# Performance work log

Measured on AMD Instinct MI355X. Metric: run time of the kernel, lower is better.

The kernel has to match this reference:

```python
import jax, jax.numpy as jnp
import numpy as np

D = 256          # descriptor_dim
H = 4            # num heads in AttentionPropagation
DH = D // H
SCALE = 0.1      # hparams['scale_factor']
THR = 0.2        # hparams['match_threshold']
NAMES = ['GATs', 'self', 'cross'] * 4


def conv1d(x, w, b):
    # 1x1 Conv1d == per-position matmul. x:[b,c,n] w:[o,c] b:[o]
    return jnp.einsum('oc,bcn->bon', w, x) + b[None, :, None]


def instnorm(x, eps=1e-5):
    # torch InstanceNorm1d (affine=False): normalize over spatial dim per channel
    mu = jnp.mean(x, axis=2, keepdims=True)
    var = jnp.var(x, axis=2, keepdims=True)
    return (x - mu) * jax.lax.rsqrt(var + eps)


def linear_attention(q, k, v):
    # q:[b,dh,h,nq] k,v:[b,dh,h,ns]
    eps = 1e-6
    q = jax.nn.elu(q) + 1.0
    k = jax.nn.elu(k) + 1.0
    m = v.shape[3]
    v = v / m
    KV = jnp.einsum('bdhm,bqhm->bqdh', k, v)
    Z = 1.0 / (jnp.einsum('bdhm,bdh->bhm', q, k.sum(3)) + eps)
    return jnp.einsum('bdhm,bqdh,bhm->bqhm', q, KV, Z) * m


def mha(x, src, pw, pb, mw, mb):
    b, _, nq = x.shape
    ns = src.shape[2]
    q = conv1d(x, pw[0], pb[0]).reshape(b, DH, H, nq)
    k = conv1d(src, pw[1], pb[1]).reshape(b, DH, H, ns)
    v = conv1d(src, pw[2], pb[2]).reshape(b, DH, H, ns)
    o = linear_attention(q, k, v).reshape(b, D, nq)
    return conv1d(o, mw, mb)


def attn_prop(x, src, pw, pb, mw, mb, w1, b1, w2, b2):
    msg = mha(x, src, pw, pb, mw, mb)
    y = jnp.concatenate([x, msg], axis=1)           # [b, 2D, n]
    y = jax.nn.relu(instnorm(conv1d(y, w1, b1)))
    return conv1d(y, w2, b2)


def gat(d2d, d3d, W, a):
    # GraphAttentionLayer (OnePose): include_self=True, additional=False,
    # with_linear_transform=True, concat=True; dropout inactive at eval.
    # d2d:[b,D,n*L] d3d:[b,D,n]
    b, _, n = d3d.shape
    x2 = jnp.transpose(d2d, (0, 2, 1)).reshape(b, n, -1, D)   # [b,n,L,D]
    x3 = jnp.transpose(d3d, (0, 2, 1))                        # [b,n,D]
    x2 = jnp.concatenate([x3[:, :, None, :], x2], axis=2)     # include self -> L+1
    Wh2 = jnp.einsum('bnld,do->bnlo', x2, W)
    Wh3 = jnp.einsum('bnd,do->bno', x3, W)
    e = jax.nn.leaky_relu(
        jnp.einsum('bno,o->bn', Wh3, a[:D])[:, :, None]
        + jnp.einsum('bnlo,o->bnl', Wh2, a[D:]), 0.2)
    att = jax.nn.softmax(e, axis=-1)
    h = jnp.einsum('bnl,bnld->bnd', att, Wh2)
    return jnp.transpose(jax.nn.elu(h), (0, 2, 1))            # [b,D,n]


def gnn_and_scores(dq, d3, d2db, projw, projb, mergew, mergeb,
                   mlp1w, mlp1b, mlp2w, mlp2b, gatW, gata, finw, finb):
    gi = 0
    ai = 0
    for name in NAMES:
        if name == 'GATs':
            d3 = gat(d2db, d3, gatW[gi], gata[gi])
            gi += 1
        else:
            src0, src1 = (d3, dq) if name == 'cross' else (dq, d3)
            p = (projw[ai], projb[ai], mergew[ai], mergeb[ai],
                 mlp1w[ai], mlp1b[ai], mlp2w[ai], mlp2b[ai])
            dq = dq + attn_prop(dq, src0, *p)
            d3 = d3 + attn_prop(d3, src1, *p)
            ai += 1
    mq = conv1d(dq, finw, finb)
    md = conv1d(d3, finw, finb)
    mq = mq / jnp.maximum(jnp.linalg.norm(mq, axis=1, keepdims=True), 1e-12)
    md = md / jnp.maximum(jnp.linalg.norm(md, axis=1, keepdims=True), 1e-12)
    scores = jnp.einsum('bdn,bdm->bnm', mq, md) / SCALE
    conf = jax.nn.softmax(scores, axis=1) * jax.nn.softmax(scores, axis=2)
    return conf


def setup_inputs() -> dict:
    key = jax.random.key(0)
    ks = jax.random.split(key, 16)
    b, n1, n2, L = 2, 3072, 3072, 8
    s = 0.02
    f32 = jnp.float32
    return {
        'desc2d_query': jax.random.normal(ks[0], (b, D, n1), f32),
        'desc3d_db': jax.random.normal(ks[1], (b, D, n2), f32),
        'desc2d_db': jax.random.normal(ks[2], (b, D, n2 * L), f32),
        'projw': jax.random.normal(ks[3], (8, 3, D, D), f32) * s,
        'projb': jnp.zeros((8, 3, D), f32),
        'mergew': jax.random.normal(ks[4], (8, D, D), f32) * s,
        'mergeb': jnp.zeros((8, D), f32),
        'mlp1w': jax.random.normal(ks[5], (8, 2 * D, 2 * D), f32) * s,
        'mlp1b': jnp.zeros((8, 2 * D), f32),
        'mlp2w': jax.random.normal(ks[6], (8, D, 2 * D), f32) * s,
        'mlp2b': jnp.zeros((8, D), f32),
        'gatW': jax.random.normal(ks[7], (4, D, D), f32) * s,
        'gata': jax.random.normal(ks[8], (4, 2 * D), f32) * s,
        'finw': jax.random.normal(ks[9], (D, D), f32) * s,
        'finb': jnp.zeros((D,), f32),
    }


def reference(desc2d_query, desc3d_db, desc2d_db, projw, projb, mergew, mergeb,
              mlp1w, mlp1b, mlp2w, mlp2b, gatW, gata, finw, finb):
    conf = gnn_and_scores(desc2d_query, desc3d_db, desc2d_db, projw, projb,
                          mergew, mergeb, mlp1w, mlp1b, mlp2w, mlp2b,
                          gatW, gata, finw, finb)
    b, n1, n2 = conf.shape
    i0 = jnp.argmax(conf, axis=2)
    m0 = jnp.max(conf, axis=2)
    i1 = jnp.argmax(conf, axis=1)
    m1 = jnp.max(conf, axis=1)
    mutual0 = jnp.arange(n1)[None] == jnp.take_along_axis(i1, i0, axis=1)
    mutual1 = jnp.arange(n2)[None] == jnp.take_along_axis(i0, i1, axis=1)
    ms0 = jnp.where(mutual0, m0, 0.0)
    ms1 = jnp.where(mutual1, jnp.take_along_axis(ms0, i1, axis=1), 0.0)
    valid0 = mutual0 & (ms0 > THR)
    valid1 = mutual1 & jnp.take_along_axis(valid0, i1, axis=1)
    ind0 = jnp.where(valid0, i0, -1)
    ind1 = jnp.where(valid1, i1, -1)
    return (ind0[0], ind1[0], ms0[0], ms1[0], conf)
```

## Files before the change

kernel.cpp:

```cpp
#include <hip/hip_runtime.h>
#include <hip/hip_bf16.h>
#include <math.h>

typedef long long ll;
typedef __attribute__((ext_vector_type(8))) short s8v;
typedef __attribute__((ext_vector_type(4))) float f4v;
typedef __attribute__((address_space(1))) unsigned int gu32;
typedef __attribute__((address_space(3))) unsigned int lu32;

#define NPOS 3072

#define OFF_STF   0LL
#define OFF_STB   3145728LL
#define OFF_QKV   4718592LL
#define OFF_MSG   9437184LL
#define OFF_HID   11010048LL
#define OFF_WBF   14155776LL
#define OFF_PBP   16941056LL
#define OFF_KV    16947200LL
#define OFF_KSUM  17012736LL
#define OFF_KSP   17013760LL
#define OFF_UVEC  17026048LL
#define OFF_E2ALL 17028096LL
#define OFF_ATT   17224704LL
#define OFF_SVEC  17280000LL
#define OFF_INP   17292288LL
#define OFF_PMAX  17300480LL
#define OFF_PSUM  17595392LL
#define OFF_CMAX  17890304LL
#define OFF_CSUM  17896448LL
#define OFF_CAPV  17902592LL
#define OFF_CAPI  17976320LL
#define OFF_I0    18050048LL
#define OFF_M0    18053120LL
#define OFF_I1    18056192LL
#define OFF_M1B   18059264LL
#define OFF_B1C   18583552LL

__device__ __forceinline__ float b2f(short s) {
  union { unsigned u; float f; } c;
  c.u = ((unsigned)(unsigned short)s) << 16;
  return c.f;
}
__device__ __forceinline__ short f2b(float f) {
  __hip_bfloat16 h = __float2bfloat16(f);
  union { __hip_bfloat16 h; short s; } c; c.h = h; return c.s;
}
__device__ __forceinline__ unsigned pk2(float a, float b) {
  return (unsigned)(unsigned short)f2b(a) | ((unsigned)(unsigned short)f2b(b) << 16);
}
__device__ __forceinline__ float waveSum(float v) {
#pragma unroll
  for (int off = 32; off > 0; off >>= 1) v += __shfl_down(v, off);
  return v;
}
__device__ __forceinline__ void gld16(const short* g, short* l) {
  __builtin_amdgcn_global_load_lds((const gu32*)g, (lu32*)l, 16, 0, 0);
}
template<int N> __device__ __forceinline__ void wvm() {
  asm volatile("s_waitcnt vmcnt(%0)" :: "n"(N) : "memory");
}
__device__ __forceinline__ void wlgk0() {
  asm volatile("s_waitcnt lgkmcnt(0)" ::: "memory");
}

template<int BI, int BJ, int KT>
__global__ __launch_bounds__(256) void bgemm_k(
    const short* __restrict__ A, const short* __restrict__ A2, int KS,
    int lda, int lda2,
    const short* __restrict__ B,
    const float* __restrict__ bias, const float* __restrict__ R,
    float* __restrict__ C, short* __restrict__ C2,
    const float* __restrict__ rs, const float* __restrict__ cs,
    int ldc, float alpha,
    ll aB, ll a2B, ll bB, ll rB, ll cB, ll c2B,
    int za, int zbo, int act, int zand)
{
  constexpr int NT = KT / 32;
  constexpr int WI = (BI == 128) ? 2 : 1;
  constexpr int JW = BJ / (4 / WI);
  constexpr int FI = (BI / WI) / 16;
  constexpr int FJ = JW / 16;
  constexpr int SA = BI / 64, SB = BJ / 64;
  constexpr int LPT = SA + SB;
  __shared__ __align__(16) short As[3][BI * 32];
  __shared__ __align__(16) short Bs[3][BJ * 32];
  const int z = blockIdx.z;
  const int zA = (z + za) & zand, zB = (z + zbo) & zand;
  const int j0 = blockIdx.x * BJ, i0 = blockIdx.y * BI;
  const int t = threadIdx.x;
  const int lane = t & 63, w = t >> 6;
  const int wi = (WI == 2) ? (w & 1) * 64 : 0;
  const int wj = (WI == 2) ? (w >> 1) * JW : w * JW;
  const int fr = lane & 15;
  const int cl = lane >> 4;
  const int r4 = cl * 4;

  const short* baseA[SA]; const short* baseA2[SA]; const short* baseB[SB];
  int slA[SA], slB[SB];
  {
    const short* Az = A + (ll)zA * aB;
    const short* A2z = A2 ? A2 + (ll)zA * a2B : nullptr;
    const short* Bz = B + (ll)zB * bB;
#pragma unroll
    for (int i = 0; i < SA; ++i) {
      int cc = t + i * 256;
      int r = cc >> 2;
      int sq = ((cc & 3) ^ ((r >> 1) & 3)) << 3;
      baseA[i] = Az + (ll)(i0 + r) * lda + sq;
      baseA2[i] = A2 ? A2z + (ll)(i0 + r) * lda2 + sq : nullptr;
      slA[i] = cc << 3;
    }
#pragma unroll
    for (int i = 0; i < SB; ++i) {
      int cc = t + i * 256;
      int r = cc >> 2;
      int sq = ((cc & 3) ^ ((r >> 1) & 3)) << 3;
      baseB[i] = Bz + (ll)(j0 + r) * KT + sq;
      slB[i] = cc << 3;
    }
  }
  int offA[FI], offB[FJ];
#pragma unroll
  for (int im = 0; im < FI; ++im) {
    int ra = wi + im * 16 + fr;
    offA[im] = ra * 32 + ((cl ^ ((ra >> 1) & 3)) << 3);
  }
#pragma unroll
  for (int in = 0; in < FJ; ++in) {
// ... 8 lines not shown
    for (int j = 0; j < FJ; ++j) acc[i][j] = (f4v)0.f;

  auto stage = [&](int tile, int bi_) {
    const int k0 = tile * 32;
    short* dA = As[bi_]; short* dB = Bs[bi_];
    if (A2 && k0 >= KS) {
#pragma unroll
      for (int i = 0; i < SA; ++i) gld16(baseA2[i] + (k0 - KS), dA + slA[i]);
    } else {
#pragma unroll
      for (int i = 0; i < SA; ++i) gld16(baseA[i] + k0, dA + slA[i]);
    }
#pragma unroll
    for (int i = 0; i < SB; ++i) gld16(baseB[i] + k0, dB + slB[i]);
  };

  stage(0, 0);
  stage(1, 1);
#pragma unroll
  for (int kt = 0; kt < NT; ++kt) {
    if (kt + 2 < NT) { stage(kt + 2, (kt + 2) % 3); wvm<2 * LPT>(); }
    else if (kt + 1 < NT) { wvm<LPT>(); }
    else { wvm<0>(); }
    __builtin_amdgcn_s_barrier();
    asm volatile("" ::: "memory");
    const short* Ac = As[kt % 3]; const short* Bc = Bs[kt % 3];
    s8v af[FI], bfr[FJ];
#pragma unroll
    for (int im = 0; im < FI; ++im) af[im] = *(const s8v*)(Ac + offA[im]);
#pragma unroll
    for (int in = 0; in < FJ; ++in) bfr[in] = *(const s8v*)(Bc + offB[in]);
#pragma unroll
    for (int im = 0; im < FI; ++im)
#pragma unroll
      for (int in = 0; in < FJ; ++in)
        acc[im][in] = __builtin_amdgcn_mfma_f32_16x16x32_bf16(
            af[im], bfr[in], acc[im][in], 0, 0, 0);
    if (kt + 1 < NT) {
      wlgk0();
      __builtin_amdgcn_s_barrier();
    }
  }

  float* Cz = C ? C + (ll)z * cB : nullptr;
  short* C2z = C2 ? C2 + (ll)z * c2B : nullptr;
  const float* Rz = R ? R + (ll)z * rB : nullptr;
  const float* rsz = rs ? rs + (ll)z * NPOS : nullptr;
  float bv4[FJ], cv4[FJ];
#pragma unroll
  for (int in = 0; in < FJ; ++in) {
    int j = j0 + wj + in * 16 + fr;
    bv4[in] = bias ? bias[j] : 0.f;
    cv4[in] = cs ? cs[(ll)zB * NPOS + j] : 1.f;
  }
#pragma unroll
  for (int im = 0; im < FI; ++im) {
#pragma unroll
    for (int r = 0; r < 4; ++r) {
      int i = i0 + wi + im * 16 + r4 + r;
      float rsv = rsz ? rsz[i] : 1.f;
      int rowo = i * ldc;
#pragma unroll
      for (int in = 0; in < FJ; ++in) {
        int j = j0 + wj + in * 16 + fr;
        float v = acc[im][in][r] * alpha;
        if (rsz) v = v * rsv * cv4[in];
        v += bv4[in];
        int off = rowo + j;
        if (Rz) v += Rz[off];
        if (act) v = v > 0.f ? v : (expf(v) - 1.f);
        if (Cz) Cz[off] = v;
        if (C2z) C2z[off] = f2b(v);
      }
    }
  }
}

__global__ void transpose_in_k(const float* __restrict__ dq, const float* __restrict__ d3,
                               float* __restrict__ stf, short* __restrict__ stb)
{
  __shared__ float tile[64][65];
  int z = blockIdx.z;
  const float* src = (z < 2) ? dq + (ll)z * 786432 : d3 + (ll)(z - 2) * 786432;
  int c0 = blockIdx.y * 64, n0 = blockIdx.x * 64;
  int t = threadIdx.x;
  int nj = t & 63, q = t >> 6;
#pragma unroll
  for (int i = 0; i < 16; ++i) {
    int ci = q + i * 4;
    tile[ci][nj] = src[(ll)(c0 + ci) * NPOS + n0 + nj];
  }
  __syncthreads();
  int cj = t & 63;
#pragma unroll
  for (int i = 0; i < 16; ++i) {
    int ni = q + i * 4;
    float v = tile[cj][ni];
    ll o = (ll)z * 786432 + (ll)(n0 + ni) * 256 + c0 + cj;
    stf[o] = v;
    stb[o] = f2b(v);
  }
}

__global__ void f2b_k(const float* __restrict__ src, short* __restrict__ dst, int n8)
{
  int gi = blockIdx.x * 256 + threadIdx.x;
  if (gi >= n8) return;
  ll e = (ll)gi * 8;
  float4 a = *(const float4*)(src + e);
  float4 b = *(const float4*)(src + e + 4);
  uint4 o;
  o.x = pk2(a.x, a.y); o.y = pk2(a.z, a.w);
  o.z = pk2(b.x, b.y); o.w = pk2(b.z, b.w);
  *(uint4*)(dst + e) = o;
}

__global__ void f2b_split_k(const float* __restrict__ src, short* __restrict__ d1,
                            short* __restrict__ d2)
{
  int gi = blockIdx.x * 256 + threadIdx.x;
  ll e = (ll)gi * 8;
  int k = (int)(e & 511);
  ll row = e >> 9;
  float4 a = *(const float4*)(src + e);
  float4 b = *(const float4*)(src + e + 4);
  uint4 o;
  o.x = pk2(a.x, a.y); o.y = pk2(a.z, a.w);
  o.z = pk2(b.x, b.y); o.w = pk2(b.z, b.w);
// ... 71 lines not shown
  int nj = t & 63, q = t >> 6;
#pragma unroll
  for (int i = 0; i < 16; ++i) {
    int di = q + i * 4;
    tile[di][nj] = src[(ll)gi * 65536 + (ll)(d0 + di) * 256 + o0 + nj];
  }
  __syncthreads();
#pragma unroll
  for (int i = 0; i < 16; ++i) {
    int oi = q + i * 4;
    dst[(ll)gi * 65536 + (ll)(o0 + oi) * 256 + d0 + nj] = f2b(tile[nj][oi]);
  }
}

__global__ void gat_prep_k(const float* __restrict__ gatW, const float* __restrict__ gata,
                           float* __restrict__ uvec)
{
  int gi = blockIdx.x; int d = threadIdx.x;
  const float* W = gatW + (ll)gi * 65536;
  const float* a = gata + gi * 512;
  float u0 = 0.f, u1 = 0.f;
  for (int o = 0; o < 256; o += 4) {
    float4 w4 = *(const float4*)(W + d * 256 + o);
    float4 a4 = *(const float4*)(a + o);
    float4 b4 = *(const float4*)(a + 256 + o);
    u0 += w4.x * a4.x + w4.y * a4.y + w4.z * a4.z + w4.w * a4.w;
    u1 += w4.x * b4.x + w4.y * b4.y + w4.z * b4.z + w4.w * b4.w;
  }
  uvec[gi * 512 + d] = u0;
  uvec[gi * 512 + 256 + d] = u1;
}

__global__ void e2all_k(const float* __restrict__ d2db, const float* __restrict__ uvec,
                        float* __restrict__ e2all)
{
  __shared__ float us[1024];
  int t = threadIdx.x;
  for (int idx = t; idx < 1024; idx += 256)
    us[idx] = uvec[(idx >> 8) * 512 + 256 + (idx & 255)];
  __syncthreads();
  int m = blockIdx.x * 256 + t;
  int b = blockIdx.y;
  const float* xb = d2db + (ll)b * 6291456;
  float a[4] = {};
  for (int c = 0; c < 256; ++c) {
    float v = xb[(ll)c * 24576 + m];
#pragma unroll
    for (int g = 0; g < 4; ++g) a[g] = fmaf(v, us[g * 256 + c], a[g]);
  }
#pragma unroll
  for (int g = 0; g < 4; ++g) e2all[((ll)g * 2 + b) * 24576 + m] = a[g];
}

__global__ void gat_att_k(const short* __restrict__ stb, const float* __restrict__ uvec,
                          const float* __restrict__ e2all, float* __restrict__ att, int gi)
{
  __shared__ float ush[512];
  int t = threadIdx.x;
  for (int idx = t; idx < 512; idx += 256) ush[idx] = uvec[gi * 512 + idx];
  __syncthreads();
  int q = t & 3, pl = t >> 2;
  int n = blockIdx.x * 64 + pl;
  int b = blockIdx.y;
  const short* xr = stb + (ll)(2 + b) * 786432 + (ll)n * 256 + q * 64;
  float a0 = 0.f, a1 = 0.f;
#pragma unroll
  for (int i = 0; i < 8; ++i) {
    s8v v8 = *(const s8v*)(xr + i * 8);
#pragma unroll
    for (int j = 0; j < 8; ++j) {
      float v = b2f(v8[j]);
      a0 = fmaf(v, ush[q * 64 + i * 8 + j], a0);
      a1 = fmaf(v, ush[256 + q * 64 + i * 8 + j], a1);
    }
  }
  a0 += __shfl_xor(a0, 1); a0 += __shfl_xor(a0, 2);
  a1 += __shfl_xor(a1, 1); a1 += __shfl_xor(a1, 2);
  if (q == 0) {
    float e[9];
    e[0] = a0 + a1;
    const float* e2b = e2all + ((ll)gi * 2 + b) * 24576 + (ll)n * 8;
#pragma unroll
    for (int l = 0; l < 8; ++l) e[l + 1] = a0 + e2b[l];
    float mx = -3.4e38f;
#pragma unroll
    for (int l = 0; l < 9; ++l) {
      e[l] = e[l] >= 0.f ? e[l] : 0.2f * e[l];
      mx = fmaxf(mx, e[l]);
    }
    float s = 0.f;
#pragma unroll
    for (int l = 0; l < 9; ++l) { e[l] = expf(e[l] - mx); s += e[l]; }
    float inv = 1.f / s;
    float* ao = att + ((ll)b * NPOS + n) * 9;
#pragma unroll
    for (int l = 0; l < 9; ++l) ao[l] = e[l] * inv;
  }
}

__global__ __launch_bounds__(256) void gat_g_k(
    const short* __restrict__ stb, const float* __restrict__ d2db,
    const float* __restrict__ att, short* __restrict__ g)
{
  __shared__ float attw[576];
  __shared__ float gtile[64 * 69];
  const int n0 = blockIdx.x * 64, c0 = blockIdx.y * 64, b = blockIdx.z;
  const int t = threadIdx.x;
  for (int idx = t; idx < 576; idx += 256)
    attw[idx] = att[((ll)b * NPOS + n0) * 9 + idx];
  __syncthreads();
  const int nl = t >> 2, l2 = (t & 3) * 2;
  for (int cc = 0; cc < 64; ++cc) {
    const float* src = d2db + ((ll)b * 256 + c0 + cc) * 24576 + (ll)n0 * 8;
    float2 v = *(const float2*)(src + t * 2);
    float p = v.x * attw[nl * 9 + 1 + l2] + v.y * attw[nl * 9 + 2 + l2];
    p += __shfl_xor(p, 1);
    p += __shfl_xor(p, 2);
    if ((t & 3) == 0) gtile[nl * 69 + cc] = p;
  }
  __syncthreads();
#pragma unroll
  for (int i = 0; i < 4; ++i) {
    int n = (t >> 4) + i * 16;
    int cp = (t & 15) * 4;
    float at0 = attw[n * 9];
    const short* dr = stb + (ll)(2 + b) * 786432 + (ll)(n0 + n) * 256 + c0 + cp;
    uint2 dv = *(const uint2*)dr;
    float d0 = b2f((short)(dv.x & 0xffff)), d1 = b2f((short)(dv.x >> 16));
    float d2 = b2f((short)(dv.y & 0xffff)), d3v = b2f((short)(dv.y >> 16));
    uint2 ov;
    ov.x = pk2(gtile[n * 69 + cp] + at0 * d0, gtile[n * 69 + cp + 1] + at0 * d1);
    ov.y = pk2(gtile[n * 69 + cp + 2] + at0 * d2, gtile[n * 69 + cp + 3] + at0 * d3v);
    *(uint2*)(g + (ll)b * 786432 + (ll)(n0 + n) * 256 + c0 + cp) = ov;
  }
}

__global__ __launch_bounds__(256) void kv_partial_k(
    const short* __restrict__ qkv, float* __restrict__ kvp, float* __restrict__ ksp)
{
  __shared__ float ks[32][66];
  __shared__ float vs[32][66];
  const int p = blockIdx.x, h = blockIdx.y, z = blockIdx.z;
  const short* base = qkv + (ll)z * 2359296;
  const int t = threadIdx.x;
  const int tq = (t >> 4) * 4, tk = (t & 15) * 4;
  const int ml = t >> 3, d8 = (t & 7) * 8;
  float acc[4][4] = {};
  float ksl = 0.f;
  for (int sub = 0; sub < 8; ++sub) {
    int m0 = p * 256 + sub * 32;
    {
      const short* kr = base + (ll)(m0 + ml) * 768 + 256 + h * 64 + d8;
      s8v k8 = *(const s8v*)kr;
      s8v v8 = *(const s8v*)(kr + 256);
#pragma unroll
      for (int j = 0; j < 8; ++j) {
        float kvv = b2f(k8[j]);
        ks[ml][d8 + j] = kvv > 0.f ? kvv + 1.f : expf(kvv);
        vs[ml][d8 + j] = b2f(v8[j]);
      }
    }
    __syncthreads();
#pragma unroll 8
    for (int mm = 0; mm < 32; ++mm) {
      float vv[4], kk[4];
#pragma unroll
      for (int i = 0; i < 4; ++i) { vv[i] = vs[mm][tq + i]; kk[i] = ks[mm][tk + i]; }
#pragma unroll
      for (int i = 0; i < 4; ++i)
#pragma unroll
        for (int j = 0; j < 4; ++j)
          acc[i][j] = fmaf(vv[i], kk[j], acc[i][j]);
    }
    if (t < 64) {
#pragma unroll 8
      for (int mm = 0; mm < 32; ++mm) ksl += ks[mm][t];
    }
    __syncthreads();
  }
  ll o = (((ll)z * 4 + h) * 12 + p) * 4096;
#pragma unroll
  for (int i = 0; i < 4; ++i)
    *(float4*)(kvp + o + (tq + i) * 64 + tk) =
        make_float4(acc[i][0], acc[i][1], acc[i][2], acc[i][3]);
  if (t < 64) ksp[(((ll)z * 4 + h) * 12 + p) * 64 + t] = ksl;
}

__global__ void kv_reduce_k(const float* __restrict__ kvp, const float* __restrict__ ksp,
                            float* __restrict__ kv, float* __restrict__ ksum)
{
  int bh = blockIdx.x; int t = threadIdx.x;
  int e0 = blockIdx.y * 1024;
  for (int e = e0 + t; e < e0 + 1024; e += 256) {
    float s = 0.f;
    for (int p = 0; p < 12; ++p) s += kvp[((ll)bh * 12 + p) * 4096 + e];
    kv[(ll)bh * 4096 + (ll)(e & 63) * 64 + (e >> 6)] = s;
  }
  if (blockIdx.y == 0 && t < 64) {
    float s = 0.f;
    for (int p = 0; p < 12; ++p) s += ksp[((ll)bh * 12 + p) * 64 + t];
    ksum[bh * 64 + t] = s;
  }
}

__global__ __launch_bounds__(256) void attn_out_k(
    const short* __restrict__ qkv, const float* __restrict__ kv,
    const float* __restrict__ ksum, short* __restrict__ obuf)
{
  __shared__ float qt[64][67];
  __shared__ float kvT[64][66];
  __shared__ float zsh[64];
  __shared__ float kss[64];
  const int n0 = blockIdx.x * 64, h = blockIdx.y, z = blockIdx.z;
  const int t = threadIdx.x;
  {
    int nl = t >> 3, d8 = (t & 7) * 8;
    const short* qr0 = qkv + (ll)z * 2359296 + (ll)(n0 + nl) * 768 + h * 64 + d8;
#pragma unroll
    for (int i = 0; i < 2; ++i) {
      const short* qr = qr0 + (ll)i * 32 * 768;
      s8v q8 = *(const s8v*)qr;
#pragma unroll
      for (int j = 0; j < 8; ++j) {
        float q = b2f(q8[j]);
        qt[nl + i * 32][d8 + j] = q > 0.f ? q + 1.f : expf(q);
      }
    }
  }
  {
    const float* kvb = kv + (ll)(z * 4 + h) * 4096;
#pragma unroll
    for (int i = 0; i < 16; ++i) {
      int idx = t + i * 256;
      kvT[idx >> 6][idx & 63] = kvb[idx];
    }
  }
  if (t < 64) kss[t] = ksum[(z * 4 + h) * 64 + t];
  __syncthreads();
  if (t < 64) {
    float s = 0.f;
    for (int d = 0; d < 64; ++d) s = fmaf(qt[t][d], kss[d], s);
    zsh[t] = 1.f / (s + 1e-6f);
  }
  __syncthreads();
  const int tn = t >> 4, tj = t & 15;
  float acc[4][4] = {};
  for (int d = 0; d < 64; ++d) {
    float av[4], bv[4];
#pragma unroll
    for (int i = 0; i < 4; ++i) av[i] = qt[tn * 4 + i][d];
    *(float4*)bv = *(const float4*)&kvT[d][tj * 4];
#pragma unroll
    for (int i = 0; i < 4; ++i)
#pragma unroll
      for (int j = 0; j < 4; ++j)
        acc[i][j] = fmaf(av[i], bv[j], acc[i][j]);
  }
#pragma unroll
  for (int i = 0; i < 4; ++i) {
    int n = n0 + tn * 4 + i;
    float zv = zsh[tn * 4 + i];
    uint2 o;
    o.x = pk2(acc[i][0] * zv, acc[i][1] * zv);
    o.y = pk2(acc[i][2] * zv, acc[i][3] * zv);
    *(uint2*)(obuf + (ll)z * 786432 + (ll)n * 256 + h * 64 + tj * 4) = o;
  }
}

__global__ void in_part_k(const short* __restrict__ hid, float* __restrict__ part)
{
  int z = blockIdx.z, cg = blockIdx.y, nc = blockIdx.x;
  int t = threadIdx.x;
  int c = cg * 64 + (t & 63);
  const short* base = hid + (ll)z * 1572864 + (ll)(nc * 384 + (t >> 6)) * 512 + c;
  float s = 0.f, q = 0.f;
#pragma unroll 4
  for (int i = 0; i < 96; ++i) {
    float v = b2f(base[(ll)i * 2048]);
    s += v; q = fmaf(v, v, q);
  }
  __shared__ float rs_[4][64], rq_[4][64];
  rs_[t >> 6][t & 63] = s; rq_[t >> 6][t & 63] = q;
  __syncthreads();
  if (t < 64) {
    s = rs_[0][t] + rs_[1][t] + rs_[2][t] + rs_[3][t];
    q = rq_[0][t] + rq_[1][t] + rq_[2][t] + rq_[3][t];
    ll o = ((((ll)z * 8 + cg) * 8 + nc) * 64 + t) * 2;
    part[o] = s; part[o + 1] = q;
  }
}

__global__ void in_apply_k(short* __restrict__ hid, const float* __restrict__ part)
{
  int z = blockIdx.z, cg = blockIdx.y, nc = blockIdx.x;
  int t = threadIdx.x;
  int c = cg * 64 + (t & 63);
  float s = 0.f, q = 0.f;
#pragma unroll
  for (int p = 0; p < 8; ++p) {
    ll o = ((((ll)z * 8 + cg) * 8 + p) * 64 + (t & 63)) * 2;
    s += part[o]; q += part[o + 1];
  }
  float mu = s * (1.f / NPOS);
  float var = q * (1.f / NPOS) - mu * mu;
  float rsig = rsqrtf(fmaxf(var, 0.f) + 1e-5f);
  short* base = hid + (ll)z * 1572864 + (ll)(nc * 384 + (t >> 6)) * 512 + c;
#pragma unroll 4
  for (int i = 0; i < 96; ++i) {
    float v = (b2f(base[(ll)i * 2048]) - mu) * rsig;
    base[(ll)i * 2048] = f2b(v > 0.f ? v : 0.f);
  }
}

__global__ void normcalc_k(const short* __restrict__ f, float* __restrict__ svec)
{
  int n = blockIdx.x * 256 + threadIdx.x;
  int z = blockIdx.y;
  const short* r = f + (ll)z * 786432 + (ll)n * 256;
  float s = 0.f;
#pragma unroll 8
  for (int i = 0; i < 32; ++i) {
    s8v v8 = *(const s8v*)(r + i * 8);
#pragma unroll
    for (int j = 0; j < 8; ++j) { float v = b2f(v8[j]); s = fmaf(v, v, s); }
  }
  svec[z * NPOS + n] = 1.f / fmaxf(sqrtf(s), 1e-12f);
}

__global__ void colstat_part_k(const float* __restrict__ S,
                               float* __restrict__ pmax, float* __restrict__ psum)
{
  int m = blockIdx.x * 256 + threadIdx.x;
  int chunk = blockIdx.y; int b = blockIdx.z;
  const float* base = S + (ll)b * 9437184 + m;
  float mx = -3.4e38f, s = 0.f;
  int n0 = chunk * 64;
  for (int n = n0; n < n0 + 64; ++n) {
    float v = base[(ll)n * NPOS];
    if (v > mx) { s = s * expf(mx - v) + 1.f; mx = v; }
    else s += expf(v - mx);
  }
  ll o = ((ll)b * 48 + chunk) * NPOS + m;
  pmax[o] = mx; psum[o] = s;
}

__global__ void colstat_comb_k(const float* __restrict__ pmax, const float* __restrict__ psum,
                               float* __restrict__ cmax, float* __restrict__ csum)
{
  int m = blockIdx.x * 256 + threadIdx.x; int b = blockIdx.y;
  float M = -3.4e38f;
  for (int c = 0; c < 48; ++c) M = fmaxf(M, pmax[((ll)b * 48 + c) * NPOS + m]);
  float s = 0.f;
  for (int c = 0; c < 48; ++c)
    s += psum[((ll)b * 48 + c) * NPOS + m] * expf(pmax[((ll)b * 48 + c) * NPOS + m] - M);
  cmax[b * NPOS + m] = M; csum[b * NPOS + m] = s;
}

__global__ __launch_bounds__(256) void rowfix_k(
    float* __restrict__ S, const float* __restrict__ cmax, const float* __restrict__ csum,
    int* __restrict__ i0, float* __restrict__ m0)
{
  int n = blockIdx.x, b = blockIdx.y, t = threadIdx.x;
  float* row = S + (ll)b * 9437184 + (ll)n * NPOS;
  __shared__ float red[4];
  float v[12];
  float mx = -3.4e38f;
#pragma unroll
  for (int i = 0; i < 12; ++i) { v[i] = row[t + i * 256]; mx = fmaxf(mx, v[i]); }
#pragma unroll
  for (int off = 32; off > 0; off >>= 1) mx = fmaxf(mx, __shfl_down(mx, off));
  if ((t & 63) == 0) red[t >> 6] = mx;
  __syncthreads();
  float rm = fmaxf(fmaxf(red[0], red[1]), fmaxf(red[2], red[3]));
  __syncthreads();
  float s = 0.f;
#pragma unroll
  for (int i = 0; i < 12; ++i) s += expf(v[i] - rm);
  s = waveSum(s);
  if ((t & 63) == 0) red[t >> 6] = s;
  __syncthreads();
  float irs = 1.f / (red[0] + red[1] + red[2] + red[3]);
  float bv = -1.f; int bi = 0;
#pragma unroll
  for (int i = 0; i < 12; ++i) {
    int m = t + i * 256;
    float f = expf(2.f * v[i] - rm - cmax[b * NPOS + m]) * irs / csum[b * NPOS + m];
    row[m] = f;
    if (f > bv) { bv = f; bi = m; }
  }
  if (b == 0) {
#pragma unroll
    for (int off = 32; off > 0; off >>= 1) {
      float ov = __shfl_down(bv, off);
      int oi = __shfl_down(bi, off);
      if (ov > bv || (ov == bv && oi < bi)) { bv = ov; bi = oi; }
    }
// ... 39 lines not shown
{
  int n = blockIdx.x * 256 + threadIdx.x;
  int j = i0[n];
  bool mut = (i1[j] == n);
  float ms0 = mut ? m0[n] : 0.f;
  bool valid = mut && (ms0 > 0.2f);
  out[n] = valid ? (float)j : -1.f;
  out[6144 + n] = ms0;
}

__global__ void match1_k(const int* __restrict__ i0, const int* __restrict__ i1,
                         float* __restrict__ out)
{
  int m = blockIdx.x * 256 + threadIdx.x;
  int j = i1[m];
  bool mut = (i0[j] == m);
  float ms0v = out[6144 + j];
  float ind0v = out[j];
  float ms1 = mut ? ms0v : 0.f;
  bool valid1 = mut && (ind0v >= 0.f);
  out[3072 + m] = valid1 ? (float)j : -1.f;
  out[9216 + m] = ms1;
}

extern "C" void kernel_launch(void* const* d_in, const int* in_sizes, int n_in,
                              void* d_out, int out_size, void* d_ws, size_t ws_size,
                              hipStream_t stream)
{
  const float* desc2dq = (const float*)d_in[0];
  const float* desc3db = (const float*)d_in[1];
  const float* desc2db = (const float*)d_in[2];
  const float* projw = (const float*)d_in[3];
  const float* projb = (const float*)d_in[4];
  const float* mergew = (const float*)d_in[5];
  const float* mergeb = (const float*)d_in[6];
  const float* mlp1w = (const float*)d_in[7];
  const float* mlp1b = (const float*)d_in[8];
  const float* mlp2w = (const float*)d_in[9];
  const float* mlp2b = (const float*)d_in[10];
  const float* gatW = (const float*)d_in[11];
  const float* gata = (const float*)d_in[12];
  const float* finw = (const float*)d_in[13];
  const float* finb = (const float*)d_in[14];

  float* ws = (float*)d_ws;
  float* out = (float*)d_out;

  float* stf = ws + OFF_STF;
  short* stb = (short*)(ws + OFF_STB);
  short* qkv = (short*)(ws + OFF_QKV);
  short* msg = (short*)(ws + OFF_MSG);
  short* obuf = msg;
  short* hid = (short*)(ws + OFF_HID);
  float* kvp = ws + OFF_HID + 1572864;
  short* wbf = (short*)(ws + OFF_WBF);
  short* projw_bf = wbf;
  short* mergewT_bf = wbf + 1572864;
  short* mlp1c_bf = wbf + 2097152;
  short* mlp2w_bf = wbf + 4194304;
  short* gatwT_bf = wbf + 5242880;
  short* finw_bf = wbf + 5505024;
  float* pbp = ws + OFF_PBP;
  float* kvb = ws + OFF_KV;
  float* ksum = ws + OFF_KSUM;
  float* ksp = ws + OFF_KSP;
  float* uvec = ws + OFF_UVEC;
  float* e2all = ws + OFF_E2ALL;
  float* att = ws + OFF_ATT;
  float* svec = ws + OFF_SVEC;
  float* inp = ws + OFF_INP;
  float* pmax = ws + OFF_PMAX;
  float* psum = ws + OFF_PSUM;
  float* cmax = ws + OFF_CMAX;
  float* csum = ws + OFF_CSUM;
  float* capv = ws + OFF_CAPV;
  int* capi = (int*)(ws + OFF_CAPI);
  int* i0 = (int*)(ws + OFF_I0);
  float* m0 = ws + OFF_M0;
  int* i1 = (int*)(ws + OFF_I1);
  short* m1b_bf = (short*)(ws + OFF_M1B);
  float* b1c = ws + OFF_B1C;
  short* finbf = msg;

  transpose_in_k<<<dim3(48, 4, 4), 256, 0, stream>>>(desc2dq, desc3db, stf, stb);
  projw_perm_k<<<6144, 256, 0, stream>>>(projw, projw_bf);
  pbp_k<<<24, 256, 0, stream>>>(projb, pbp);
  mergewT_k<<<dim3(4, 4, 8), 256, 0, stream>>>(mergew, mergewT_bf);
  f2b_split_k<<<1024, 256, 0, stream>>>(mlp1w, mlp1c_bf, m1b_bf);
  f2b_k<<<512, 256, 0, stream>>>(mlp2w, mlp2w_bf, 131072);
  gatw_t_k<<<dim3(4, 4, 4), 256, 0, stream>>>(gatW, gatwT_bf);
  f2b_k<<<32, 256, 0, stream>>>(finw, finw_bf, 8192);
  biasfold_k<<<64, 256, 0, stream>>>(mlp1w, mlp1b, mergeb, b1c);
  bgemm_k<64, 128, 256><<<dim3(2, 8, 8), 256, 0, stream>>>(
      m1b_bf, nullptr, 0, 256, 0, mergewT_bf, nullptr, nullptr,
      nullptr, mlp1c_bf + 256, nullptr, nullptr,
      512, 1.f, 131072, 0, 65536, 0, 0, 262144, 0, 0, 0, 7);
  gat_prep_k<<<4, 256, 0, stream>>>(gatW, gata, uvec);
  e2all_k<<<dim3(96, 2), 256, 0, stream>>>(desc2db, uvec, e2all);

  auto attn_layer = [&](int ai, int cross) {
    const short* pw = projw_bf + (ll)ai * 196608;
    const float* pb = pbp + (ll)ai * 768;
    if (!cross) {
      bgemm_k<64, 128, 256><<<dim3(6, 48, 4), 256, 0, stream>>>(
          stb, nullptr, 0, 256, 0, pw, pb, nullptr, nullptr, qkv, nullptr, nullptr,
          768, 1.f, 786432, 0, 0, 0, 0, 2359296, 0, 0, 0, 3);
    } else {
      bgemm_k<64, 64, 256><<<dim3(4, 48, 4), 256, 0, stream>>>(
          stb, nullptr, 0, 256, 0, pw, pb, nullptr, nullptr, qkv, nullptr, nullptr,
          768, 1.f, 786432, 0, 0, 0, 0, 2359296, 0, 0, 0, 3);
      bgemm_k<64, 128, 256><<<dim3(4, 48, 4), 256, 0, stream>>>(
          stb, nullptr, 0, 256, 0, pw + 65536, pb + 256, nullptr, nullptr, qkv + 256,
          nullptr, nullptr,
          768, 1.f, 786432, 0, 0, 0, 0, 2359296, 2, 0, 0, 3);
    }
    kv_partial_k<<<dim3(12, 4, 4), 256, 0, stream>>>(qkv, kvp, ksp);
    kv_reduce_k<<<dim3(16, 4), 256, 0, stream>>>(kvp, ksp, kvb, ksum);
    attn_out_k<<<dim3(48, 4, 4), 256, 0, stream>>>(qkv, kvb, ksum, obuf);
    bgemm_k<64, 128, 512><<<dim3(4, 48, 4), 256, 0, stream>>>(
        stb, obuf, 256, 256, 256, mlp1c_bf + (ll)ai * 262144, b1c + (ll)ai * 512,
        nullptr, nullptr, hid, nullptr, nullptr,
        512, 1.f, 786432, 786432, 0, 0, 0, 1572864, 0, 0, 0, 3);
    in_part_k<<<dim3(8, 8, 4), 256, 0, stream>>>(hid, inp);
    in_apply_k<<<dim3(8, 8, 4), 256, 0, stream>>>(hid, inp);
    bgemm_k<64, 64, 512><<<dim3(4, 48, 4), 256, 0, stream>>>(
        hid, nullptr, 0, 512, 0, mlp2w_bf + (ll)ai * 131072, mlp2b + (ll)ai * 256,
        stf, stf, stb, nullptr, nullptr,
        256, 1.f, 1572864, 0, 0, 786432, 786432, 786432, 0, 0, 0, 3);
  };

  auto gat_layer = [&](int gi) {
    gat_att_k<<<dim3(48, 2), 256, 0, stream>>>(stb, uvec, e2all, att, gi);
    gat_g_k<<<dim3(48, 4, 2), 256, 0, stream>>>(stb, desc2db, att, obuf);
    bgemm_k<64, 64, 256><<<dim3(4, 48, 2), 256, 0, stream>>>(
        obuf, nullptr, 0, 256, 0, gatwT_bf + (ll)gi * 65536, nullptr, nullptr,
        stf + (ll)2 * 786432, stb + (ll)2 * 786432, nullptr, nullptr,
        256, 1.f, 786432, 0, 0, 0, 786432, 786432, 0, 0, 1, 3);
  };

  int ai = 0, gi = 0;
  for (int r = 0; r < 4; ++r) {
    gat_layer(gi); gi++;
    attn_layer(ai, 0); ai++;
    attn_layer(ai, 1); ai++;
  }

  bgemm_k<64, 64, 256><<<dim3(4, 48, 4), 256, 0, stream>>>(
      stb, nullptr, 0, 256, 0, finw_bf, finb, nullptr, nullptr, finbf, nullptr, nullptr,
      256, 1.f, 786432, 0, 0, 0, 0, 786432, 0, 0, 0, 3);
  normcalc_k<<<dim3(12, 4), 256, 0, stream>>>(finbf, svec);

  float* conf = out + 12288;
  bgemm_k<64, 128, 256><<<dim3(24, 48, 2), 256, 0, stream>>>(
      finbf, nullptr, 0, 256, 0, finbf, nullptr, nullptr, conf, nullptr, svec, svec,
      3072, 10.f, 786432, 0, 786432, 0, 9437184, 0, 0, 2, 0, 3);

  colstat_part_k<<<dim3(12, 48, 2), 256, 0, stream>>>(conf, pmax, psum);
  colstat_comb_k<<<dim3(12, 2), 256, 0, stream>>>(pmax, psum, cmax, csum);
  rowfix_k<<<dim3(NPOS, 2), 256, 0, stream>>>(conf, cmax, csum, i0, m0);
  colamax_part_k<<<dim3(12, 24), 256, 0, stream>>>(conf, capv, capi);
  colamax_comb_k<<<12, 256, 0, stream>>>(capv, capi, i1);
  match0_k<<<12, 256, 0, stream>>>(i0, m0, i1, out);
  match1_k<<<12, 256, 0, stream>>>(i0, i1, out);
}
```

Before: 1.526 ms.

## Fuse reductions into GEMM epilogues and replace partial-reduce kernels with atomics

Adds an epilogue mode to the bf16 GEMM so it also produces column online-softmax partials (conf GEMM), instance-norm sums and sums of squares (mlp1 GEMM), and row squared norms (final projection). This removes the separate colstat_part, in_part, normcalc and kv_reduce passes over large buffers. It also folds GAT attention weights into gat_g_k and makes kv_partial accumulate with atomics into pre-zeroed per-layer buffers. The cost is atomic contention, a few extra epilogue registers, and nondeterministic float summation order.

```diff
diff --git a/kernel.cpp b/kernel.cpp
--- a/kernel.cpp
+++ b/kernel.cpp
@@ -17,14 +17,8 @@
 #define OFF_HID   11010048LL
 #define OFF_WBF   14155776LL
 #define OFF_PBP   16941056LL
-#define OFF_KV    16947200LL
-#define OFF_KSUM  17012736LL
-#define OFF_KSP   17013760LL
 #define OFF_UVEC  17026048LL
 #define OFF_E2ALL 17028096LL
-#define OFF_ATT   17224704LL
-#define OFF_SVEC  17280000LL
-#define OFF_INP   17292288LL
 #define OFF_PMAX  17300480LL
 #define OFF_PSUM  17595392LL
 #define OFF_CMAX  17890304LL
@@ -36,6 +30,11 @@
 #define OFF_I1    18056192LL
 #define OFF_M1B   18059264LL
 #define OFF_B1C   18583552LL
+#define OFF_INAT  18587648LL
+#define OFF_SVSQ  18620416LL
+#define OFF_KVAT  18632704LL
+#define OFF_KSAT  19156992LL
+#define ZERO_N    577536LL
 
 __device__ __forceinline__ float b2f(short s) {
   union { unsigned u; float f; } c;
@@ -64,7 +63,7 @@
   asm volatile("s_waitcnt lgkmcnt(0)" ::: "memory");
 }
 
-template<int BI, int BJ, int KT>
+template<int BI, int BJ, int KT, int SMODE>
 __global__ __launch_bounds__(256) void bgemm_k(
     const short* __restrict__ A, const short* __restrict__ A2, int KS,
     int lda, int lda2,
@@ -74,7 +73,8 @@
     const float* __restrict__ rs, const float* __restrict__ cs,
     int ldc, float alpha,
     ll aB, ll a2B, ll bB, ll rB, ll cB, ll c2B,
-    int za, int zbo, int act, int zand)
+    int za, int zbo, int act, int zand,
+    float* __restrict__ sp0, float* __restrict__ sp1, int rsmode)
 {
   constexpr int NT = KT / 32;
   constexpr int WI = (BI == 128) ? 2 : 1;
@@ -189,14 +189,21 @@
     int j = j0 + wj + in * 16 + fr;
     bv4[in] = bias ? bias[j] : 0.f;
     cv4[in] = cs ? cs[(ll)zB * NPOS + j] : 1.f;
-  }
+    if (rsmode) cv4[in] = 1.f / fmaxf(sqrtf(cv4[in]), 1e-12f);
+  }
+  float stM[FJ], stS[FJ], stQ[FJ];
+#pragma unroll
+  for (int in = 0; in < FJ; ++in) { stM[in] = -3.4e38f; stS[in] = 0.f; stQ[in] = 0.f; }
+
 #pragma unroll
   for (int im = 0; im < FI; ++im) {
 #pragma unroll
     for (int r = 0; r < 4; ++r) {
       int i = i0 + wi + im * 16 + r4 + r;
       float rsv = rsz ? rsz[i] : 1.f;
+      if (rsmode) rsv = 1.f / fmaxf(sqrtf(rsv), 1e-12f);
       int rowo = i * ldc;
+      float rq3 = 0.f;
 #pragma unroll
       for (int in = 0; in < FJ; ++in) {
         int j = j0 + wj + in * 16 + fr;
@@ -206,11 +213,64 @@
         int off = rowo + j;
         if (Rz) v += Rz[off];
         if (act) v = v > 0.f ? v : (expf(v) - 1.f);
+        if constexpr (SMODE == 1) {
+          float m = stM[in];
+          if (v > m) { stS[in] = stS[in] * expf(m - v) + 1.f; stM[in] = v; }
+          else stS[in] += expf(v - m);
+        }
+        if constexpr (SMODE == 2) { stS[in] += v; stQ[in] = fmaf(v, v, stQ[in]); }
+        if constexpr (SMODE == 3) rq3 = fmaf(v, v, rq3);
         if (Cz) Cz[off] = v;
         if (C2z) C2z[off] = f2b(v);
       }
-    }
-  }
+      if constexpr (SMODE == 3) {
+        rq3 += __shfl_xor(rq3, 1);
+        rq3 += __shfl_xor(rq3, 2);
+        rq3 += __shfl_xor(rq3, 4);
+        rq3 += __shfl_xor(rq3, 8);
+        if (fr == 0) atomicAdd(&sp0[(ll)z * NPOS + i], rq3);
+      }
+    }
+  }
+  if constexpr (SMODE == 1) {
+    const ll totj = (ll)gridDim.x * BJ;
+#pragma unroll
+    for (int in = 0; in < FJ; ++in) {
+      float m = stM[in], s = stS[in];
+#pragma unroll
+      for (int d = 16; d <= 32; d <<= 1) {
+        float mo = __shfl_xor(m, d);
+        float so = __shfl_xor(s, d);
+        float M = fmaxf(m, mo);
+        s = s * expf(m - M) + so * expf(mo - M);
+        m = M;
+      }
+      if (cl == 0) {
+        ll o = ((ll)z * gridDim.y + blockIdx.y) * totj + (j0 + wj + in * 16 + fr);
+        sp0[o] = m; sp1[o] = s;
+      }
+    }
+  }
+  if constexpr (SMODE == 2) {
+    const ll totj = (ll)gridDim.x * BJ;
+#pragma unroll
+    for (int in = 0; in < FJ; ++in) {
+      float s = stS[in], q = stQ[in];
+      s += __shfl_xor(s, 16); s += __shfl_xor(s, 32);
+      q += __shfl_xor(q, 16); q += __shfl_xor(q, 32);
+      if (cl == 0) {
+        ll o = ((ll)z * totj + (j0 + wj + in * 16 + fr)) * 2;
+        atomicAdd(&sp0[o], s);
+        atomicAdd(&sp0[o + 1], q);
+      }
+    }
+  }
+}
+
+__global__ void zero_k(float* __restrict__ p, int n)
+{
+  int i = blockIdx.x * 1024 + threadIdx.x * 4;
+  if (i < n) *(float4*)(p + i) = make_float4(0.f, 0.f, 0.f, 0.f);
 }
 
 __global__ void transpose_in_k(const float* __restrict__ dq, const float* __restrict__ d3,
@@ -388,62 +448,55 @@
   for (int g = 0; g < 4; ++g) e2all[((ll)g * 2 + b) * 24576 + m] = a[g];
 }
 
-__global__ void gat_att_k(const short* __restrict__ stb, const float* __restrict__ uvec,
-                          const float* __restrict__ e2all, float* __restrict__ att, int gi)
-{
-  __shared__ float ush[512];
-  int t = threadIdx.x;
-  for (int idx = t; idx < 512; idx += 256) ush[idx] = uvec[gi * 512 + idx];
-  __syncthreads();
-  int q = t & 3, pl = t >> 2;
-  int n = blockIdx.x * 64 + pl;
-  int b = blockIdx.y;
-  const short* xr = stb + (ll)(2 + b) * 786432 + (ll)n * 256 + q * 64;
-  float a0 = 0.f, a1 = 0.f;
-#pragma unroll
-  for (int i = 0; i < 8; ++i) {
-    s8v v8 = *(const s8v*)(xr + i * 8);
-#pragma unroll
-    for (int j = 0; j < 8; ++j) {
-      float v = b2f(v8[j]);
-      a0 = fmaf(v, ush[q * 64 + i * 8 + j], a0);
-      a1 = fmaf(v, ush[256 + q * 64 + i * 8 + j], a1);
-    }
-  }
-  a0 += __shfl_xor(a0, 1); a0 += __shfl_xor(a0, 2);
-  a1 += __shfl_xor(a1, 1); a1 += __shfl_xor(a1, 2);
-  if (q == 0) {
-    float e[9];
-    e[0] = a0 + a1;
-    const float* e2b = e2all + ((ll)gi * 2 + b) * 24576 + (ll)n * 8;
-#pragma unroll
-    for (int l = 0; l < 8; ++l) e[l + 1] = a0 + e2b[l];
-    float mx = -3.4e38f;
-#pragma unroll
-    for (int l = 0; l < 9; ++l) {
-      e[l] = e[l] >= 0.f ? e[l] : 0.2f * e[l];
-      mx = fmaxf(mx, e[l]);
-    }
-    float s = 0.f;
-#pragma unroll
-    for (int l = 0; l < 9; ++l) { e[l] = expf(e[l] - mx); s += e[l]; }
-    float inv = 1.f / s;
-    float* ao = att + ((ll)b * NPOS + n) * 9;
-#pragma unroll
-    for (int l = 0; l < 9; ++l) ao[l] = e[l] * inv;
-  }
-}
-
 __global__ __launch_bounds__(256) void gat_g_k(
     const short* __restrict__ stb, const float* __restrict__ d2db,
-    const float* __restrict__ att, short* __restrict__ g)
-{
+    const float* __restrict__ uvec, const float* __restrict__ e2all,
+    short* __restrict__ g, int gi)
+{
+  __shared__ float ush[512];
   __shared__ float attw[576];
   __shared__ float gtile[64 * 69];
   const int n0 = blockIdx.x * 64, c0 = blockIdx.y * 64, b = blockIdx.z;
   const int t = threadIdx.x;
-  for (int idx = t; idx < 576; idx += 256)
-    attw[idx] = att[((ll)b * NPOS + n0) * 9 + idx];
+  for (int idx = t; idx < 512; idx += 256) ush[idx] = uvec[gi * 512 + idx];
+  __syncthreads();
+  {
+    const int q = t & 3, pl = t >> 2;
+    const int n = n0 + pl;
+    const short* xr = stb + (ll)(2 + b) * 786432 + (ll)n * 256 + q * 64;
+    float a0 = 0.f, a1 = 0.f;
+#pragma unroll
+    for (int i = 0; i < 8; ++i) {
+      s8v v8 = *(const s8v*)(xr + i * 8);
+#pragma unroll
+      for (int j = 0; j < 8; ++j) {
+        float v = b2f(v8[j]);
+        a0 = fmaf(v, ush[q * 64 + i * 8 + j], a0);
+        a1 = fmaf(v, ush[256 + q * 64 + i * 8 + j], a1);
+      }
+    }
+    a0 += __shfl_xor(a0, 1); a0 += __shfl_xor(a0, 2);
+    a1 += __shfl_xor(a1, 1); a1 += __shfl_xor(a1, 2);
+    if (q == 0) {
+      float e[9];
+      e[0] = a0 + a1;
+      const float* e2b = e2all + ((ll)gi * 2 + b) * 24576 + (ll)n * 8;
+#pragma unroll
+      for (int l = 0; l < 8; ++l) e[l + 1] = a0 + e2b[l];
+      float mx = -3.4e38f;
+#pragma unroll
+      for (int l = 0; l < 9; ++l) {
+        e[l] = e[l] >= 0.f ? e[l] : 0.2f * e[l];
+        mx = fmaxf(mx, e[l]);
+      }
+      float s = 0.f;
+#pragma unroll
+      for (int l = 0; l < 9; ++l) { e[l] = expf(e[l] - mx); s += e[l]; }
+      float inv = 1.f / s;
+#pragma unroll
+      for (int l = 0; l < 9; ++l) attw[pl * 9 + l] = e[l] * inv;
+    }
+  }
   __syncthreads();
   const int nl = t >> 2, l2 = (t & 3) * 2;
   for (int cc = 0; cc < 64; ++cc) {
@@ -472,7 +525,7 @@
 }
 
 __global__ __launch_bounds__(256) void kv_partial_k(
-    const short* __restrict__ qkv, float* __restrict__ kvp, float* __restrict__ ksp)
+    const short* __restrict__ qkv, float* __restrict__ kvat, float* __restrict__ ksat)
 {
   __shared__ float ks[32][66];
   __shared__ float vs[32][66];
@@ -514,29 +567,13 @@
     }
     __syncthreads();
   }
-  ll o = (((ll)z * 4 + h) * 12 + p) * 4096;
+  float* kvz = kvat + ((ll)z * 4 + h) * 4096;
 #pragma unroll
   for (int i = 0; i < 4; ++i)
-    *(float4*)(kvp + o + (tq + i) * 64 + tk) =
-        make_float4(acc[i][0], acc[i][1], acc[i][2], acc[i][3]);
-  if (t < 64) ksp[(((ll)z * 4 + h) * 12 + p) * 64 + t] = ksl;
-}
-
-__global__ void kv_reduce_k(const float* __restrict__ kvp, const float* __restrict__ ksp,
-                            float* __restrict__ kv, float* __restrict__ ksum)
-{
-  int bh = blockIdx.x; int t = threadIdx.x;
-  int e0 = blockIdx.y * 1024;
-  for (int e = e0 + t; e < e0 + 1024; e += 256) {
-    float s = 0.f;
-    for (int p = 0; p < 12; ++p) s += kvp[((ll)bh * 12 + p) * 4096 + e];
-    kv[(ll)bh * 4096 + (ll)(e & 63) * 64 + (e >> 6)] = s;
-  }
-  if (blockIdx.y == 0 && t < 64) {
-    float s = 0.f;
-    for (int p = 0; p < 12; ++p) s += ksp[((ll)bh * 12 + p) * 64 + t];
-    ksum[bh * 64 + t] = s;
-  }
+#pragma unroll
+    for (int j = 0; j < 4; ++j)
+      atomicAdd(&kvz[(tk + j) * 64 + tq + i], acc[i][j]);
+  if (t < 64) atomicAdd(&ksat[(z * 4 + h) * 64 + t], ksl);
 }
 
 __global__ __launch_bounds__(256) void attn_out_k(
@@ -603,42 +640,14 @@
   }
 }
 
-__global__ void in_part_k(const short* __restrict__ hid, float* __restrict__ part)
+__global__ void in_apply_k(short* __restrict__ hid, const float* __restrict__ inat)
 {
   int z = blockIdx.z, cg = blockIdx.y, nc = blockIdx.x;
   int t = threadIdx.x;
   int c = cg * 64 + (t & 63);
-  const short* base = hid + (ll)z * 1572864 + (ll)(nc * 384 + (t >> 6)) * 512 + c;
-  float s = 0.f, q = 0.f;
-#pragma unroll 4
-  for (int i = 0; i < 96; ++i) {
-    float v = b2f(base[(ll)i * 2048]);
-    s += v; q = fmaf(v, v, q);
-  }
-  __shared__ float rs_[4][64], rq_[4][64];
-  rs_[t >> 6][t & 63] = s; rq_[t >> 6][t & 63] = q;
-  __syncthreads();
-  if (t < 64) {
-    s = rs_[0][t] + rs_[1][t] + rs_[2][t] + rs_[3][t];
-    q = rq_[0][t] + rq_[1][t] + rq_[2][t] + rq_[3][t];
-    ll o = ((((ll)z * 8 + cg) * 8 + nc) * 64 + t) * 2;
-    part[o] = s; part[o + 1] = q;
-  }
-}
-
-__global__ void in_apply_k(short* __restrict__ hid, const float* __restrict__ part)
-{
-  int z = blockIdx.z, cg = blockIdx.y, nc = blockIdx.x;
-  int t = threadIdx.x;
-  int c = cg * 64 + (t & 63);
-  float s = 0.f, q = 0.f;
-#pragma unroll
-  for (int p = 0; p < 8; ++p) {
-    ll o = ((((ll)z * 8 + cg) * 8 + p) * 64 + (t & 63)) * 2;
-    s += part[o]; q += part[o + 1];
-  }
-  float mu = s * (1.f / NPOS);
-  float var = q * (1.f / NPOS) - mu * mu;
+  float2 sq = *(const float2*)(inat + ((ll)(z * 512 + c) << 1));
+  float mu = sq.x * (1.f / NPOS);
+  float var = sq.y * (1.f / NPOS) - mu * mu;
   float rsig = rsqrtf(fmaxf(var, 0.f) + 1e-5f);
   short* base = hid + (ll)z * 1572864 + (ll)(nc * 384 + (t >> 6)) * 512 + c;
 #pragma unroll 4
@@ -646,38 +655,6 @@
     float v = (b2f(base[(ll)i * 2048]) - mu) * rsig;
     base[(ll)i * 2048] = f2b(v > 0.f ? v : 0.f);
   }
-}
-
-__global__ void normcalc_k(const short* __restrict__ f, float* __restrict__ svec)
-{
-  int n = blockIdx.x * 256 + threadIdx.x;
-  int z = blockIdx.y;
-  const short* r = f + (ll)z * 786432 + (ll)n * 256;
-  float s = 0.f;
-#pragma unroll 8
-  for (int i = 0; i < 32; ++i) {
-    s8v v8 = *(const s8v*)(r + i * 8);
-#pragma unroll
-    for (int j = 0; j < 8; ++j) { float v = b2f(v8[j]); s = fmaf(v, v, s); }
-  }
-  svec[z * NPOS + n] = 1.f / fmaxf(sqrtf(s), 1e-12f);
-}
-
-__global__ void colstat_part_k(const float* __restrict__ S,
-                               float* __restrict__ pmax, float* __restrict__ psum)
-{
-  int m = blockIdx.x * 256 + threadIdx.x;
-  int chunk = blockIdx.y; int b = blockIdx.z;
-  const float* base = S + (ll)b * 9437184 + m;
-  float mx = -3.4e38f, s = 0.f;
-  int n0 = chunk * 64;
-  for (int n = n0; n < n0 + 64; ++n) {
-    float v = base[(ll)n * NPOS];
-    if (v > mx) { s = s * expf(mx - v) + 1.f; mx = v; }
-    else s += expf(v - mx);
-  }
-  ll o = ((ll)b * 48 + chunk) * NPOS + m;
-  pmax[o] = mx; psum[o] = s;
 }
 
 __global__ void colstat_comb_k(const float* __restrict__ pmax, const float* __restrict__ psum,
@@ -823,7 +800,6 @@
   short* msg = (short*)(ws + OFF_MSG);
   short* obuf = msg;
   short* hid = (short*)(ws + OFF_HID);
-  float* kvp = ws + OFF_HID + 1572864;
   short* wbf = (short*)(ws + OFF_WBF);
   short* projw_bf = wbf;
   short* mergewT_bf = wbf + 1572864;
@@ -832,14 +808,8 @@
   short* gatwT_bf = wbf + 5242880;
   short* finw_bf = wbf + 5505024;
   float* pbp = ws + OFF_PBP;
-  float* kvb = ws + OFF_KV;
-  float* ksum = ws + OFF_KSUM;
-  float* ksp = ws + OFF_KSP;
   float* uvec = ws + OFF_UVEC;
   float* e2all = ws + OFF_E2ALL;
-  float* att = ws + OFF_ATT;
-  float* svec = ws + OFF_SVEC;
-  float* inp = ws + OFF_INP;
   float* pmax = ws + OFF_PMAX;
   float* psum = ws + OFF_PSUM;
   float* cmax = ws + OFF_CMAX;
@@ -851,8 +821,13 @@
   int* i1 = (int*)(ws + OFF_I1);
   short* m1b_bf = (short*)(ws + OFF_M1B);
   float* b1c = ws + OFF_B1C;
+  float* inat = ws + OFF_INAT;
+  float* svsq = ws + OFF_SVSQ;
+  float* kvat = ws + OFF_KVAT;
+  float* ksat = ws + OFF_KSAT;
   short* finbf = msg;
 
+  zero_k<<<564, 256, 0, stream>>>(inat, (int)ZERO_N);
   transpose_in_k<<<dim3(48, 4, 4), 256, 0, stream>>>(desc2dq, desc3db, stf, stb);
   projw_perm_k<<<6144, 256, 0, stream>>>(projw, projw_bf);
   pbp_k<<<24, 256, 0, stream>>>(projb, pbp);
@@ -862,10 +837,11 @@
   gatw_t_k<<<dim3(4, 4, 4), 256, 0, stream>>>(gatW, gatwT_bf);
   f2b_k<<<32, 256, 0, stream>>>(finw, finw_bf, 8192);
   biasfold_k<<<64, 256, 0, stream>>>(mlp1w, mlp1b, mergeb, b1c);
-  bgemm_k<64, 128, 256><<<dim3(2, 8, 8), 256, 0, stream>>>(
+  bgemm_k<64, 128, 256, 0><<<dim3(2, 8, 8), 256, 0, stream>>>(
       m1b_bf, nullptr, 0, 256, 0, mergewT_bf, nullptr, nullptr,
       nullptr, mlp1c_bf + 256, nullptr, nullptr,
-      512, 1.f, 131072, 0, 65536, 0, 0, 262144, 0, 0, 0, 7);
+      512, 1.f, 131072, 0, 65536, 0, 0, 262144, 0, 0, 0, 7,
+      nullptr, nullptr, 0);
   gat_prep_k<<<4, 256, 0, stream>>>(gatW, gata, uvec);
   e2all_k<<<dim3(96, 2), 256, 0, stream>>>(desc2db, uvec, e2all);
 
@@ -873,40 +849,45 @@
     const short* pw = projw_bf + (ll)ai * 196608;
     const float* pb = pbp + (ll)ai * 768;
     if (!cross) {
-      bgemm_k<64, 128, 256><<<dim3(6, 48, 4), 256, 0, stream>>>(
+      bgemm_k<64, 128, 256, 0><<<dim3(6, 48, 4), 256, 0, stream>>>(
           stb, nullptr, 0, 256, 0, pw, pb, nullptr, nullptr, qkv, nullptr, nullptr,
-          768, 1.f, 786432, 0, 0, 0, 0, 2359296, 0, 0, 0, 3);
+          768, 1.f, 786432, 0, 0, 0, 0, 2359296, 0, 0, 0, 3,
+          nullptr, nullptr, 0);
     } else {
-      bgemm_k<64, 64, 256><<<dim3(4, 48, 4), 256, 0, stream>>>(
+      bgemm_k<64, 64, 256, 0><<<dim3(4, 48, 4), 256, 0, stream>>>(
           stb, nullptr, 0, 256, 0, pw, pb, nullptr, nullptr, qkv, nullptr, nullptr,
-          768, 1.f, 786432, 0, 0, 0, 0, 2359296, 0, 0, 0, 3);
-      bgemm_k<64, 128, 256><<<dim3(4, 48, 4), 256, 0, stream>>>(
+          768, 1.f, 786432, 0, 0, 0, 0, 2359296, 0, 0, 0, 3,
+          nullptr, nullptr, 0);
+      bgemm_k<64, 128, 256, 0><<<dim3(4, 48, 4), 256, 0, stream>>>(
           stb, nullptr, 0, 256, 0, pw + 65536, pb + 256, nullptr, nullptr, qkv + 256,
           nullptr, nullptr,
-          768, 1.f, 786432, 0, 0, 0, 0, 2359296, 2, 0, 0, 3);
-    }
-    kv_partial_k<<<dim3(12, 4, 4), 256, 0, stream>>>(qkv, kvp, ksp);
-    kv_reduce_k<<<dim3(16, 4), 256, 0, stream>>>(kvp, ksp, kvb, ksum);
-    attn_out_k<<<dim3(48, 4, 4), 256, 0, stream>>>(qkv, kvb, ksum, obuf);
-    bgemm_k<64, 128, 512><<<dim3(4, 48, 4), 256, 0, stream>>>(
+          768, 1.f, 786432, 0, 0, 0, 0, 2359296, 2, 0, 0, 3,
+          nullptr, nullptr, 0);
+    }
+    kv_partial_k<<<dim3(12, 4, 4), 256, 0, stream>>>(
+        qkv, kvat + (ll)ai * 65536, ksat + (ll)ai * 1024);
+    attn_out_k<<<dim3(48, 4, 4), 256, 0, stream>>>(
+        qkv, kvat + (ll)ai * 65536, ksat + (ll)ai * 1024, obuf);
+    bgemm_k<64, 128, 512, 2><<<dim3(4, 48, 4), 256, 0, stream>>>(
         stb, obuf, 256, 256, 256, mlp1c_bf + (ll)ai * 262144, b1c + (ll)ai * 512,
         nullptr, nullptr, hid, nullptr, nullptr,
-        512, 1.f, 786432, 786432, 0, 0, 0, 1572864, 0, 0, 0, 3);
-    in_part_k<<<dim3(8, 8, 4), 256, 0, stream>>>(hid, inp);
-    in_apply_k<<<dim3(8, 8, 4), 256, 0, stream>>>(hid, inp);
-    bgemm_k<64, 64, 512><<<dim3(4, 48, 4), 256, 0, stream>>>(
+        512, 1.f, 786432, 786432, 0, 0, 0, 1572864, 0, 0, 0, 3,
+        inat + (ll)ai * 4096, nullptr, 0);
+    in_apply_k<<<dim3(8, 8, 4), 256, 0, stream>>>(hid, inat + (ll)ai * 4096);
+    bgemm_k<64, 64, 512, 0><<<dim3(4, 48, 4), 256, 0, stream>>>(
         hid, nullptr, 0, 512, 0, mlp2w_bf + (ll)ai * 131072, mlp2b + (ll)ai * 256,
         stf, stf, stb, nullptr, nullptr,
-        256, 1.f, 1572864, 0, 0, 786432, 786432, 786432, 0, 0, 0, 3);
+        256, 1.f, 1572864, 0, 0, 786432, 786432, 786432, 0, 0, 0, 3,
+        nullptr, nullptr, 0);
   };
 
   auto gat_layer = [&](int gi) {
-    gat_att_k<<<dim3(48, 2), 256, 0, stream>>>(stb, uvec, e2all, att, gi);
-    gat_g_k<<<dim3(48, 4, 2), 256, 0, stream>>>(stb, desc2db, att, obuf);
-    bgemm_k<64, 64, 256><<<dim3(4, 48, 2), 256, 0, stream>>>(
+    gat_g_k<<<dim3(48, 4, 2), 256, 0, stream>>>(stb, desc2db, uvec, e2all, obuf, gi);
+    bgemm_k<64, 64, 256, 0><<<dim3(4, 48, 2), 256, 0, stream>>>(
         obuf, nullptr, 0, 256, 0, gatwT_bf + (ll)gi * 65536, nullptr, nullptr,
         stf + (ll)2 * 786432, stb + (ll)2 * 786432, nullptr, nullptr,
-        256, 1.f, 786432, 0, 0, 0, 786432, 786432, 0, 0, 1, 3);
+        256, 1.f, 786432, 0, 0, 0, 786432, 786432, 0, 0, 1, 3,
+        nullptr, nullptr, 0);
   };
 
   int ai = 0, gi = 0;
@@ -916,17 +897,17 @@
     attn_layer(ai, 1); ai++;
   }
 
-  bgemm_k<64, 64, 256><<<dim3(4, 48, 4), 256, 0, stream>>>(
+  bgemm_k<64, 64, 256, 3><<<dim3(4, 48, 4), 256, 0, stream>>>(
       stb, nullptr, 0, 256, 0, finw_bf, finb, nullptr, nullptr, finbf, nullptr, nullptr,
-      256, 1.f, 786432, 0, 0, 0, 0, 786432, 0, 0, 0, 3);
-  normcalc_k<<<dim3(12, 4), 256, 0, stream>>>(finbf, svec);
+      256, 1.f, 786432, 0, 0, 0, 0, 786432, 0, 0, 0, 3,
+      svsq, nullptr, 0);
 
   float* conf = out + 12288;
-  bgemm_k<64, 128, 256><<<dim3(24, 48, 2), 256, 0, stream>>>(
-      finbf, nullptr, 0, 256, 0, finbf, nullptr, nullptr, conf, nullptr, svec, svec,
-      3072, 10.f, 786432, 0, 786432, 0, 9437184, 0, 0, 2, 0, 3);
-
-  colstat_part_k<<<dim3(12, 48, 2), 256, 0, stream>>>(conf, pmax, psum);
+  bgemm_k<64, 128, 256, 1><<<dim3(24, 48, 2), 256, 0, stream>>>(
+      finbf, nullptr, 0, 256, 0, finbf, nullptr, nullptr, conf, nullptr, svsq, svsq,
+      3072, 10.f, 786432, 0, 786432, 0, 9437184, 0, 0, 2, 0, 3,
+      pmax, psum, 1);
+
   colstat_comb_k<<<dim3(12, 2), 256, 0, stream>>>(pmax, psum, cmax, csum);
   rowfix_k<<<dim3(NPOS, 2), 256, 0, stream>>>(conf, cmax, csum, i0, m0);
   colamax_part_k<<<dim3(12, 24), 256, 0, stream>>>(conf, capv, capi);
```

Result: no change. 1.523 ms (-0.2%).
